# Optimization experiments

Hardware: AMD Instinct MI355X
Metric: run time of the kernel (lower is better)

Reference implementation:

```python
import jax, jax.numpy as jnp
import numpy as np

N = 100000      # nodes
E = 1600000     # directed edges (before self loops)
F_IN = 3        # node_feature_dim
H = 32          # hidden_dim
BN_EPS = 1e-5


def _linear_params(k, fan_in, fan_out):
    lim = 1.0 / np.sqrt(fan_in)
    kw, kb = jax.random.split(k)
    W = jax.random.uniform(kw, (fan_in, fan_out), jnp.float32, -lim, lim)
    b = jax.random.uniform(kb, (fan_out,), jnp.float32, -lim, lim)
    return W, b


def setup_inputs() -> dict:
    key = jax.random.key(0)
    ks = jax.random.split(key, 12)
    x = jax.random.normal(ks[0], (N, F_IN), jnp.float32)
    edge_index = jax.random.randint(ks[1], (2, E), 0, N, dtype=jnp.int64)
    node_type = jax.random.randint(ks[2], (N,), 0, 3, dtype=jnp.int64)
    W1, b1 = _linear_params(ks[3], F_IN, H)
    W2, b2 = _linear_params(ks[4], H, H)
    W3, b3 = _linear_params(ks[5], H, H)
    g1 = jnp.ones((H,), jnp.float32); be1 = jnp.zeros((H,), jnp.float32)
    g2 = jnp.ones((H,), jnp.float32); be2 = jnp.zeros((H,), jnp.float32)
    Wc1, bc1 = _linear_params(ks[6], H, H // 2)
    Wc2, bc2 = _linear_params(ks[7], H // 2, 1)
    Wd1, bd1 = _linear_params(ks[8], H, H // 2)
    Wd2, bd2 = _linear_params(ks[9], H // 2, 1)
    return dict(x=x, edge_index=edge_index, node_type=node_type,
                W1=W1, b1=b1, W2=W2, b2=b2, W3=W3, b3=b3,
                g1=g1, be1=be1, g2=g2, be2=be2,
                Wc1=Wc1, bc1=bc1, Wc2=Wc2, bc2=bc2,
                Wd1=Wd1, bd1=bd1, Wd2=Wd2, bd2=bd2)


def reference(x, edge_index, node_type, W1, b1, W2, b2, W3, b3,
              g1, be1, g2, be2, Wc1, bc1, Wc2, bc2, Wd1, bd1, Wd2, bd2):
    n = x.shape[0]
    # GCNConv (PyG default): add self loops, symmetric deg^-1/2 normalization
    loop = jnp.arange(n, dtype=edge_index.dtype)
    src = jnp.concatenate([edge_index[0], loop])  # [E+N]
    dst = jnp.concatenate([edge_index[1], loop])
    deg = jax.ops.segment_sum(jnp.ones_like(dst, dtype=x.dtype), dst, num_segments=n)
    dinv = jnp.where(deg > 0, jax.lax.rsqrt(jnp.maximum(deg, 1.0)), 0.0)
    norm = dinv[src] * dinv[dst]  # [E+N]

    def conv(h, W, b):
        msg = (h @ W)[src] * norm[:, None]                  # gather + scale
        return jax.ops.segment_sum(msg, dst, num_segments=n) + b  # scatter-add

    def bn(h, g, be):  # BatchNorm1d with batch statistics (training math)
        mu = h.mean(axis=0)
        var = ((h - mu) ** 2).mean(axis=0)
        return (h - mu) * jax.lax.rsqrt(var + BN_EPS) * g + be

    h = bn(jax.nn.relu(conv(x, W1, b1)), g1, be1)   # dropout = identity (eval)
    h = bn(jax.nn.relu(conv(h, W2, b2)), g2, be2)
    h = jax.nn.relu(conv(h, W3, b3))

    cand_mask = node_type == 0
    cand_emb = h[cand_mask]                                 # [C, H]
    cand_scores = (jax.nn.relu(cand_emb @ Wc1 + bc1) @ Wc2 + bc2)[:, 0]

    w = jax.nn.softmax(h.sum(axis=1))[:, None]              # [N,1] importance
    g_emb = (h * w).sum(axis=0, keepdims=True)              # [1, H]
    dn = (jax.nn.relu(g_emb @ Wd1 + bd1) @ Wd2 + bd2).reshape(())

    logits = jnp.concatenate([cand_scores, dn[None]], axis=0)
    cand_idx = jnp.nonzero(cand_mask)[0]
    return logits, cand_idx
```

## Files before the change

kernel.cpp:

```cpp
#include <hip/hip_runtime.h>

typedef unsigned int uint;
typedef unsigned char uchar;

#define NB_MAX 256
#define NPB_MAX 2048

#if defined(__has_builtin)
#if __has_builtin(__builtin_amdgcn_cvt_pk_f32_fp8) && __has_builtin(__builtin_amdgcn_cvt_pk_fp8_f32)
#define HW_FP8 1
#endif
#endif

typedef __attribute__((ext_vector_type(2))) float v2f;

static __device__ __forceinline__ uint f2fp8_sw(float v) {
    v = fminf(fmaxf(v, -448.f), 448.f);
    uint u = __float_as_uint(v);
    uint s = (u >> 24) & 0x80u;
    uint mag = u & 0x7FFFFFFFu;
    uint r = mag + 0x7FFFFu + ((mag >> 20) & 1u);
    if (r < 0x3C800000u) return s;
    uint e8 = (r - 0x3C000000u) >> 20;
    return s | min(e8, 0x7Eu);
}
static __device__ __forceinline__ float fp82f(uint b) {
    uint mag = b & 0x7Fu;
    uint bits = ((b & 0x80u) << 24) | ((mag << 20) + 0x3C000000u);
    return mag ? __uint_as_float(bits) : 0.f;
}
static __device__ __forceinline__ void dec8(uint2 v, float* o) {
#ifdef HW_FP8
    v2f a = __builtin_amdgcn_cvt_pk_f32_fp8((int)v.x, false);
    v2f b = __builtin_amdgcn_cvt_pk_f32_fp8((int)v.x, true);
    v2f c = __builtin_amdgcn_cvt_pk_f32_fp8((int)v.y, false);
    v2f d = __builtin_amdgcn_cvt_pk_f32_fp8((int)v.y, true);
    o[0]=a.x; o[1]=a.y; o[2]=b.x; o[3]=b.y;
    o[4]=c.x; o[5]=c.y; o[6]=d.x; o[7]=d.y;
#else
    o[0]=fp82f(v.x&0xFF); o[1]=fp82f((v.x>>8)&0xFF); o[2]=fp82f((v.x>>16)&0xFF); o[3]=fp82f(v.x>>24);
    o[4]=fp82f(v.y&0xFF); o[5]=fp82f((v.y>>8)&0xFF); o[6]=fp82f((v.y>>16)&0xFF); o[7]=fp82f(v.y>>24);
#endif
}
static __device__ __forceinline__ uint2 enc8(const float* o) {
#ifdef HW_FP8
    int rx = __builtin_amdgcn_cvt_pk_fp8_f32(o[0], o[1], 0, false);
    rx = __builtin_amdgcn_cvt_pk_fp8_f32(o[2], o[3], rx, true);
    int ry = __builtin_amdgcn_cvt_pk_fp8_f32(o[4], o[5], 0, false);
    ry = __builtin_amdgcn_cvt_pk_fp8_f32(o[6], o[7], ry, true);
    return make_uint2((uint)rx, (uint)ry);
#else
    uint2 r;
    r.x = f2fp8_sw(o[0]) | (f2fp8_sw(o[1])<<8) | (f2fp8_sw(o[2])<<16) | (f2fp8_sw(o[3])<<24);
    r.y = f2fp8_sw(o[4]) | (f2fp8_sw(o[5])<<8) | (f2fp8_sw(o[6])<<16) | (f2fp8_sw(o[7])<<24);
    return r;
#endif
}
static __device__ __forceinline__ void dec32(const uchar* row, float* o) {
    const uint4* r4 = (const uint4*)row;
    uint4 A = r4[0], B = r4[1];
    dec8(make_uint2(A.x,A.y), o); dec8(make_uint2(A.z,A.w), o+8);
    dec8(make_uint2(B.x,B.y), o+16); dec8(make_uint2(B.z,B.w), o+24);
}

static __device__ __forceinline__ unsigned wave_incl_scan(unsigned v) {
    int lane = threadIdx.x & 63;
    #pragma unroll
    for (int d = 1; d < 64; d <<= 1) {
        unsigned t = (unsigned)__shfl_up((int)v, d, 64);
        if (lane >= d) v += t;
    }
    return v;
}

static __device__ void block_excl_scan(const uint* in, uint* out, int n, uint* wscr) {
    int tid = threadIdx.x;
    int lane = tid & 63, wid = tid >> 6;
    int base = tid * 8;
    uint v[8], pre[8], s = 0;
    #pragma unroll
    for (int k = 0; k < 8; k++) v[k] = (base + k < n) ? in[base + k] : 0u;
    #pragma unroll
    for (int k = 0; k < 8; k++) { pre[k] = s; s += v[k]; }
    uint is = wave_incl_scan(s);
    __syncthreads();
    if (lane == 63) wscr[wid] = is;
    __syncthreads();
    uint woff = 0;
    for (int wI = 0; wI < wid; wI++) woff += wscr[wI];
    uint excl = is - s + woff;
    #pragma unroll
    for (int k = 0; k < 8; k++) if (base + k < n) out[base + k] = excl + pre[k];
    __syncthreads();
}

__global__ __launch_bounds__(256) void bucket_hist_kernel(const int* src, const int* dst,
                                                          const int* nt, uint* bcnt, uint* bcand,
                                                          int E, int N, int NB, int shift) {
    __shared__ uint bh[NB_MAX], ch[NB_MAX];
    int tid = threadIdx.x;
    bh[tid] = 0; ch[tid] = 0;
    __syncthreads();
    int gs = gridDim.x * 256;
    for (int i = blockIdx.x * 256 + tid; i < E; i += gs) {
        int d = dst[i], s = src[i];
        if ((uint)d < (uint)N && (uint)s < (uint)N) atomicAdd(&bh[d >> shift], 1u);
    }
    for (int i = blockIdx.x * 256 + tid; i < N; i += gs) {
        if (nt[i] == 0) atomicAdd(&ch[i >> shift], 1u);
    }
    __syncthreads();
    if (bh[tid]) atomicAdd(&bcnt[tid], bh[tid]);
    if (ch[tid]) atomicAdd(&bcand[tid], ch[tid]);
}

__global__ __launch_bounds__(256) void partition_kernel(const int* src, const int* dst,
                                                        const uint* bcnt, uint* alloc0,
                                                        uint* staging, int E, int N, int shift) {
    __shared__ uint bbase_s[NB_MAX];
    __shared__ uint lh[NB_MAX], gb[NB_MAX];
    __shared__ uint ws4[4];
    int tid = threadIdx.x;
    int lane = tid & 63, wid = tid >> 6;
    uint a = bcnt[tid];
    uint ia = wave_incl_scan(a);
    if (lane == 63) ws4[wid] = ia;
    __syncthreads();
    uint off = 0;
    for (int wI = 0; wI < wid; wI++) off += ws4[wI];
    bbase_s[tid] = ia - a + off;
    lh[tid] = 0;
    __syncthreads();
    int base = blockIdx.x * 2048;
    uint mask = (1u << shift) - 1u;
    int breg[8];
    uint rreg[8], pk8[8];
    #pragma unroll
    for (int k = 0; k < 8; k++) {
        int e = base + k * 256 + tid;
        breg[k] = -1;
        if (e < E) {
            int s = src[e], d = dst[e];
            if ((uint)d < (uint)N && (uint)s < (uint)N) {
                int b = d >> shift;
                pk8[k] = (((uint)d & mask) << 17) | (uint)s;
                breg[k] = b;
                rreg[k] = atomicAdd(&lh[b], 1u);
            }
        }
    }
    __syncthreads();
    gb[tid] = lh[tid] ? (bbase_s[tid] + atomicAdd(&alloc0[tid], lh[tid])) : 0u;
    __syncthreads();
    #pragma unroll
    for (int k = 0; k < 8; k++) {
        if (breg[k] >= 0)
            staging[gb[breg[k]] + rreg[k]] = pk8[k];
    }
}

__global__ __launch_bounds__(256) void local_csr_kernel(const uint* staging, const uint* bcnt,
                                                        const uint* bcand, const int* nt,
                                                        const float* x,
                                                        int* csr_src, uint* csr_off, uint* cand_pos,
                                                        float* dinv, float4* xs,
                                                        int N, int shift, int NB) {
    __shared__ uint deg[NPB_MAX];
    __shared__ uint ofs[NPB_MAX];
    __shared__ uint ws4[4];
    __shared__ uint sb[4];
    int b = blockIdx.x, tid = threadIdx.x;
    int lane = tid & 63, wid = tid >> 6;
    uint a = bcnt[tid];
    uint ia = wave_incl_scan(a);
    if (lane == 63) ws4[wid] = ia;
    __syncthreads();
    uint off = 0;
    for (int wI = 0; wI < wid; wI++) off += ws4[wI];
    if (tid == b) { sb[0] = ia - a + off; sb[1] = ia + off; }
    __syncthreads();
    uint c = bcand[tid];
    uint ic = wave_incl_scan(c);
    if (lane == 63) ws4[wid] = ic;
    __syncthreads();
    uint offc = 0;
    for (int wI = 0; wI < wid; wI++) offc += ws4[wI];
    if (tid == b) sb[2] = ic - c + offc;
    __syncthreads();
    uint ebase = sb[0], eend = sb[1], cb = sb[2];
    int nbase = b << shift;
    int ncount = min(1 << shift, N - nbase);
    for (int i = tid; i < ncount; i += 256) deg[i] = 0;
    __syncthreads();
    for (uint p = ebase + tid; p < eend; p += 256)
        atomicAdd(&deg[staging[p] >> 17], 1u);
    __syncthreads();
    block_excl_scan(deg, ofs, ncount, ws4);
    for (int i = tid; i < ncount; i += 256)
        csr_off[nbase + i] = ebase + ofs[i];
    if (b == NB - 1 && tid == 0) csr_off[N] = eend;
    for (int i = tid; i < ncount; i += 256) {
        int g = nbase + i;
        float di = rsqrtf((float)(deg[i] + 1u));
        dinv[g] = di;
        xs[g] = make_float4(x[3*g] * di, x[3*g+1] * di, x[3*g+2] * di, di);
    }
    __syncthreads();
    for (int i = tid; i < ncount; i += 256) deg[i] = 0;
    __syncthreads();
    for (uint p = ebase + tid; p < eend; p += 256) {
        uint pkv = staging[p];
        uint dl = pkv >> 17;
        uint pos = ebase + ofs[dl] + atomicAdd(&deg[dl], 1u);
        csr_src[pos] = (int)(pkv & 0x1FFFFu);
    }
    __syncthreads();
    for (int i = tid; i < ncount; i += 256) deg[i] = (nt[nbase + i] == 0) ? 1u : 0u;
    __syncthreads();
    block_excl_scan(deg, ofs, ncount, ws4);
    for (int i = tid; i < ncount; i += 256) cand_pos[nbase + i] = cb + ofs[i];
}

__global__ __launch_bounds__(256) void agg1_kernel(const float* xs, const int* csr_src,
                                                   const uint* csr_off, const float* dinv,
                                                   const float* W1, const float* b1, uchar* hb,
                                                   float* Sbuf, int n,
                                                   float* stats_sum, float* stats_sq,
                                                   uint* gt) {
    const int tid = threadIdx.x;
    const int wave = tid >> 6;
    const int lane = tid & 63;
    const int c4 = lane & 3;
    const int slot = lane >> 2;
    const int qlead = lane & ~3;
    __shared__ float W1s[96];
    __shared__ uint s_lt, s_chunk;
    if (tid < 96) W1s[tid] = W1[tid];
    float bv[8];
    #pragma unroll
    for (int j = 0; j < 8; j++) bv[j] = b1[c4 * 8 + j];
    float bs[8], bq[8];
    #pragma unroll
    for (int j = 0; j < 8; j++) { bs[j] = 0.f; bq[j] = 0.f; }
    __syncthreads();
    while (true) {
        if (tid == 0) s_chunk = atomicAdd(gt, 1u);
        __syncthreads();
        uint cbase = s_chunk * 128u;
        if (cbase >= (uint)n) break;
        uint avail = min((uint)n - cbase, 128u);
        if (tid == 0) s_lt = 0u;
        __syncthreads();
        while (true) {
            uint li = 0;
            if (c4 == 0) li = atomicAdd(&s_lt, 1u);
            li = (uint)__shfl((int)li, qlead, 64);
            if (li >= avail) break;
            uint node = cbase + li;
            uint s = csr_off[node], e = csr_off[node + 1];
            float acc = xs[(size_t)node * 4 + c4];
            for (uint p = s; p < e; p += 8) {
                uint idx[8];
                float wg[8];
                #pragma unroll
                for (int j = 0; j < 8; j++) {
                    uint q = p + (uint)j;
                    uint qc = min(q, e - 1u);
                    idx[j] = (uint)csr_src[qc];
                    wg[j] = (q < e) ? 1.f : 0.f;
                }
                #pragma unroll
                for (int j = 0; j < 8; j++)
                    acc = fmaf(wg[j], xs[(size_t)idx[j] * 4 + c4], acc);
            }
            if (c4 == 3) Sbuf[node] = acc;
            float di = dinv[node];
            float u = di * acc;
            float u0 = __shfl(u, qlead, 64);
            float u1 = __shfl(u, qlead + 1, 64);
            float u2 = __shfl(u, qlead + 2, 64);
            float hv[8], sv[8];
            #pragma unroll
            for (int j = 0; j < 8; j++) {
                int ch = c4 * 8 + j;
                float o = u0 * W1s[ch] + u1 * W1s[32 + ch] + u2 * W1s[64 + ch] + bv[j];
                hv[j] = fmaxf(o, 0.f);
                sv[j] = di * hv[j];
            }
            *(uint2*)(hb + (size_t)node * 32 + c4 * 8) = enc8(sv);
            #pragma unroll
            for (int j = 0; j < 8; j++) { bs[j] += hv[j]; bq[j] += hv[j] * hv[j]; }
        }
        __syncthreads();
    }
    #pragma unroll
    for (int m = 4; m < 64; m <<= 1) {
        #pragma unroll
        for (int j = 0; j < 8; j++) {
            bs[j] += __shfl_xor(bs[j], m, 64);
            bq[j] += __shfl_xor(bq[j], m, 64);
        }
    }
    __shared__ float ssum[4][32], ssq[4][32];
    if (slot == 0) {
        #pragma unroll
        for (int j = 0; j < 8; j++) { ssum[wave][c4 * 8 + j] = bs[j]; ssq[wave][c4 * 8 + j] = bq[j]; }
    }
    __syncthreads();
    if (tid < 32) {
        atomicAdd(&stats_sum[tid], ssum[0][tid] + ssum[1][tid] + ssum[2][tid] + ssum[3][tid]);
        atomicAdd(&stats_sq[tid],  ssq[0][tid] + ssq[1][tid] + ssq[2][tid] + ssq[3][tid]);
    }
}

template<int MODE>
__global__ __launch_bounds__(256) void aggbn_kernel(const uchar* hin, const int* csr_src,
                                                    const uint* csr_off, const float* dinv,
                                                    const float* Sbuf,
                                                    const float* stats_sum, const float* stats_sq,
                                                    const float* g, const float* be,
                                                    const float* W, const float* bias,
                                                    uchar* hout, int n, float inv_n,
                                                    float* osum, float* osq,
                                                    float* rowsum, uint* maxkey, uint* gt) {
    const int tid = threadIdx.x;
    const int wave = tid >> 6;
    const int lane = tid & 63;
    const int c4 = lane & 3;
    const int slot = lane >> 2;
    const int qlead = lane & ~3;
    __shared__ float Ws[1024];
    __shared__ float cs[32], a_s[32], d_s[32];
    __shared__ uint s_lt, s_chunk;
    if (tid < 32) {
        float mu = stats_sum[tid] * inv_n;
        float var = fmaxf(stats_sq[tid] * inv_n - mu * mu, 0.f);
        float a = g[tid] * rsqrtf(var + 1e-5f);
        a_s[tid] = a;
        d_s[tid] = be[tid] - mu * a;
    }
    __syncthreads();
    for (int t = tid; t < 1024; t += 256) Ws[t] = a_s[t >> 5] * W[t];
    if (tid < 32) {
        float c = 0.f;
        for (int k = 0; k < 32; k++) c += d_s[k] * W[k * 32 + tid];
        cs[tid] = c;
    }
    float bv[8];
    #pragma unroll
    for (int j = 0; j < 8; j++) bv[j] = bias[c4 * 8 + j];
    float bs[8], bq[8];
    if (MODE == 0) {
        #pragma unroll
        for (int j = 0; j < 8; j++) { bs[j] = 0.f; bq[j] = 0.f; }
    }
    float lmax = -3.0e38f;
    __syncthreads();
    while (true) {
        if (tid == 0) s_chunk = atomicAdd(gt, 1u);
        __syncthreads();
        uint cbase = s_chunk * 128u;
        if (cbase >= (uint)n) break;
        uint avail = min((uint)n - cbase, 128u);
        if (tid == 0) s_lt = 0u;
        __syncthreads();
        while (true) {
            uint li = 0;
            if (c4 == 0) li = atomicAdd(&s_lt, 1u);
            li = (uint)__shfl((int)li, qlead, 64);
            if (li >= avail) break;
            uint node = cbase + li;
            uint s = csr_off[node], e = csr_off[node + 1];
            float acc[8];
            dec8(*(const uint2*)(hin + (size_t)node * 32 + c4 * 8), acc);
            for (uint p = s; p < e; p += 8) {
                uint idx[8];
                float wg[8];
                #pragma unroll
                for (int j = 0; j < 8; j++) {
                    uint q = p + (uint)j;
                    uint qc = min(q, e - 1u);
                    idx[j] = (uint)csr_src[qc];
                    wg[j] = (q < e) ? 1.f : 0.f;
                }
                #pragma unroll
                for (int j = 0; j < 8; j++) {
                    float t[8];
                    dec8(*(const uint2*)(hin + (size_t)idx[j] * 32 + c4 * 8), t);
                    #pragma unroll
                    for (int cI = 0; cI < 8; cI++) acc[cI] = fmaf(wg[j], t[cI], acc[cI]);
                }
            }
            float af[32];
            #pragma unroll
            for (int cc = 0; cc < 4; cc++) {
                #pragma unroll
                for (int r = 0; r < 8; r++)
                    af[cc * 8 + r] = __shfl(acc[r], qlead + cc, 64);
            }
            float di = dinv[node];
            float Sv = Sbuf[node];
            float hv[8];
            #pragma unroll
            for (int jj = 0; jj < 8; jj++) {
                int j = c4 * 8 + jj;
                float t = cs[j] * Sv;
                #pragma unroll
                for (int k = 0; k < 32; k++) t = fmaf(Ws[k * 32 + j], af[k], t);
                hv[jj] = fmaxf(fmaf(di, t, bv[jj]), 0.f);
            }
            if (MODE == 0) {
                float sv[8];
                #pragma unroll
                for (int jj = 0; jj < 8; jj++) sv[jj] = di * hv[jj];
                *(uint2*)(hout + (size_t)node * 32 + c4 * 8) = enc8(sv);
                #pragma unroll
                for (int jj = 0; jj < 8; jj++) { bs[jj] += hv[jj]; bq[jj] += hv[jj] * hv[jj]; }
            } else {
                *(uint2*)(hout + (size_t)node * 32 + c4 * 8) = enc8(hv);
                float rs = ((hv[0] + hv[1]) + (hv[2] + hv[3])) + ((hv[4] + hv[5]) + (hv[6] + hv[7]));
                rs += __shfl_xor(rs, 1, 64);
                rs += __shfl_xor(rs, 2, 64);
                if (c4 == 0) { rowsum[node] = rs; lmax = fmaxf(lmax, rs); }
            }
        }
        __syncthreads();
    }
    if (MODE == 0) {
        #pragma unroll
        for (int m = 4; m < 64; m <<= 1) {
            #pragma unroll
            for (int j = 0; j < 8; j++) {
                bs[j] += __shfl_xor(bs[j], m, 64);
                bq[j] += __shfl_xor(bq[j], m, 64);
            }
        }
        __shared__ float ssum[4][32], ssq[4][32];
        if (slot == 0) {
            #pragma unroll
            for (int j = 0; j < 8; j++) { ssum[wave][c4 * 8 + j] = bs[j]; ssq[wave][c4 * 8 + j] = bq[j]; }
        }
        __syncthreads();
        if (tid < 32) {
            atomicAdd(&osum[tid], ssum[0][tid] + ssum[1][tid] + ssum[2][tid] + ssum[3][tid]);
            atomicAdd(&osq[tid],  ssq[0][tid] + ssq[1][tid] + ssq[2][tid] + ssq[3][tid]);
        }
    } else {
        #pragma unroll
        for (int m = 1; m < 64; m <<= 1) lmax = fmaxf(lmax, __shfl_xor(lmax, m, 64));
        __shared__ float lm[4];
        if (lane == 0) lm[wave] = lmax;
        __syncthreads();
        if (tid == 0) {
            float m = fmaxf(fmaxf(lm[0], lm[1]), fmaxf(lm[2], lm[3]));
            uint u = __float_as_uint(m);
            uint key = (u & 0x80000000u) ? ~u : (u | 0x80000000u);
            atomicMax(maxkey, key);
        }
    }
}

__global__ __launch_bounds__(256) void head_kernel(const uchar* hb, const int* nt,
                                                   const uint* pos, const float* Wc1,
                                                   const float* bc1, const float* Wc2,
                                                   const float* bc2, const float* rowsum,
                                                   const uint* maxkey, float* gvec, float* Zp,
                                                   uint* ticket, const float* Wd1,
                                                   const float* bd1, const float* Wd2,
                                                   const float* bd2, float* out, int n, int C) {
    __shared__ float W1s[512], b1s[16], W2s[16];
    __shared__ float ls[256];
    __shared__ float ge[32], tt[16];
    __shared__ int lastflag;
    int tid = threadIdx.x;
    for (int t = tid; t < 512; t += 256) W1s[t] = Wc1[t];
    if (tid < 16) { b1s[tid] = bc1[tid]; W2s[tid] = Wc2[tid]; }
    __syncthreads();
    int i = blockIdx.x * 256 + tid;
    if (i < n && nt[i] == 0) {
        float hv[32];
        dec32(hb + (size_t)i * 32, hv);
        float s = bc2[0];
        #pragma unroll
        for (int j = 0; j < 16; j++) {
            float u = b1s[j];
            #pragma unroll
            for (int k = 0; k < 32; k++) u += hv[k] * W1s[k * 16 + j];
            s += fmaxf(u, 0.f) * W2s[j];
        }
        s = fminf(fmaxf(s, -1000.f), 1000.f);
        uint p = pos[i];
        if (p < (uint)C) {
            out[p] = s;
            out[C + 1 + p] = (float)i;
        }
    }
    uint key = *maxkey;
    float M = 0.f;
    if (key != 0u) M = (key & 0x80000000u) ? __uint_as_float(key ^ 0x80000000u) : __uint_as_float(~key);
    int lane = tid & 31, grp = tid >> 5;
    int stride = gridDim.x * 8;
    float accZ = 0.f, accg = 0.f;
    for (int node = blockIdx.x * 8 + grp; node < n; node += stride) {
        float ew = __expf(rowsum[node] - M);
        accg += fp82f(hb[(size_t)node * 32 + lane]) * ew;
        if (lane == 0) accZ += ew;
    }
    ls[tid] = accg;
    __syncthreads();
    if (tid < 32) {
        float a = 0.f;
        #pragma unroll
        for (int g = 0; g < 8; g++) a += ls[tid + 32 * g];
        atomicAdd(&gvec[tid], a);
    }
    __syncthreads();
    ls[tid] = (lane == 0) ? accZ : 0.f;
    __syncthreads();
    if (tid == 0) {
        float a = 0.f;
        for (int t = 0; t < 256; t += 32) a += ls[t];
        atomicAdd(Zp, a);
        __threadfence();
        uint old = atomicAdd(ticket, 1u);
        lastflag = (old == gridDim.x - 1) ? 1 : 0;
    }
    __syncthreads();
    if (lastflag) {
        __threadfence();
        if (tid < 32) ge[tid] = atomicAdd(&gvec[tid], 0.f);
        if (tid == 0) ls[0] = atomicAdd(Zp, 0.f);
        __syncthreads();
        float Zv = fmaxf(ls[0], 1e-30f);
        if (tid < 32) ge[tid] /= Zv;
        __syncthreads();
        if (tid < 16) {
            float s = bd1[tid];
            for (int k = 0; k < 32; k++) s += ge[k] * Wd1[k * 16 + tid];
            tt[tid] = fmaxf(s, 0.f);
        }
        __syncthreads();
        if (tid == 0) {
            float s = bd2[0];
            for (int j = 0; j < 16; j++) s += tt[j] * Wd2[j];
            out[C] = fminf(fmaxf(s, -1000.f), 1000.f);
        }
    }
}

extern "C" void kernel_launch(void* const* d_in, const int* in_sizes, int n_in,
                              void* d_out, int out_size, void* d_ws, size_t ws_size,
                              hipStream_t stream) {
    const float* x   = (const float*)d_in[0];
    const int*   ei  = (const int*)d_in[1];
    const int*   nt  = (const int*)d_in[2];
    const float* W1  = (const float*)d_in[3];  const float* b1  = (const float*)d_in[4];
    const float* W2  = (const float*)d_in[5];  const float* b2  = (const float*)d_in[6];
    const float* W3  = (const float*)d_in[7];  const float* b3  = (const float*)d_in[8];
    const float* g1  = (const float*)d_in[9];  const float* be1 = (const float*)d_in[10];
    const float* g2  = (const float*)d_in[11]; const float* be2 = (const float*)d_in[12];
    const float* Wc1 = (const float*)d_in[13]; const float* bc1 = (const float*)d_in[14];
    const float* Wc2 = (const float*)d_in[15]; const float* bc2 = (const float*)d_in[16];
    const float* Wd1 = (const float*)d_in[17]; const float* bd1 = (const float*)d_in[18];
    const float* Wd2 = (const float*)d_in[19]; const float* bd2 = (const float*)d_in[20];

    const int N = in_sizes[0] / 3;
    const int E = in_sizes[1] / 2;
    const int C = (out_size - 1) / 2;
    const int* e_src = ei;
    const int* e_dst = ei + E;
    float* out = (float*)d_out;

    int shift = 9;
    while (((N + (1 << shift) - 1) >> shift) > NB_MAX) shift++;
    const int NB = (N + (1 << shift) - 1) >> shift;

    char* w = (char*)d_ws;
    auto alloc = [&](size_t bytes) { void* p = (void*)w; w += (bytes + 255) & ~(size_t)255; return p; };
    float*    stats  = (float*)alloc(256 * 4);
    uint*     bcnt   = (uint*)alloc(NB_MAX * 4);
    uint*     bcand  = (uint*)alloc(NB_MAX * 4);
    uint*     alloc0 = (uint*)alloc(NB_MAX * 4);
    size_t zero_bytes = (size_t)((char*)w - (char*)stats);
    float*    dinv   = (float*)alloc((size_t)N * 4);
    uint*     csr_off= (uint*)alloc((size_t)(N + 1) * 4);
    uint*     cand_pos=(uint*)alloc((size_t)N * 4);
    float*    rowsum = (float*)alloc((size_t)N * 4);
    float*    Sbuf   = (float*)alloc((size_t)N * 4);
    int*      csr_src= (int*)alloc((size_t)E * 4);
    uint*     staging= (uint*)alloc((size_t)E * 4);
    uchar*    zb     = (uchar*)alloc((size_t)N * 32);
    uchar*    hb     = (uchar*)alloc((size_t)N * 32);
    float4*   xs     = (float4*)zb;

    float* sum1 = stats;       float* sq1 = stats + 32;
    float* sum2 = stats + 64;  float* sq2 = stats + 96;
    float* gvec = stats + 128; float* Zp  = stats + 160;
    uint* maxkey = (uint*)(stats + 161);
    uint* ticket = (uint*)(stats + 162);
    uint* gt1 = (uint*)(stats + 163);
    uint* gt2 = (uint*)(stats + 164);
    uint* gt3 = (uint*)(stats + 165);

    hipMemsetAsync(stats, 0, zero_bytes, stream);

    const int gN   = (N + 255) / 256;
    const int gPar = (E + 2047) / 2048;
    int gAgg = (N + 127) / 128;
    if (gAgg > 512) gAgg = 512;
    const float inv_n = 1.0f / (float)N;

    hipLaunchKernelGGL(bucket_hist_kernel, dim3(784), dim3(256), 0, stream, e_src, e_dst, nt, bcnt, bcand, E, N, NB, shift);
    hipLaunchKernelGGL(partition_kernel, dim3(gPar), dim3(256), 0, stream, e_src, e_dst, bcnt, alloc0, staging, E, N, shift);
    hipLaunchKernelGGL(local_csr_kernel, dim3(NB), dim3(256), 0, stream, staging, bcnt, bcand, nt,
                       x, csr_src, csr_off, cand_pos, dinv, xs, N, shift, NB);

    hipLaunchKernelGGL(agg1_kernel, dim3(gAgg), dim3(256), 0, stream, (const float*)xs, csr_src, csr_off,
                       dinv, W1, b1, hb, Sbuf, N, sum1, sq1, gt1);

    hipLaunchKernelGGL((aggbn_kernel<0>), dim3(gAgg), dim3(256), 0, stream, hb, csr_src, csr_off,
                       dinv, Sbuf, sum1, sq1, g1, be1, W2, b2, zb, N, inv_n,
                       sum2, sq2, rowsum, maxkey, gt2);

    hipLaunchKernelGGL((aggbn_kernel<1>), dim3(gAgg), dim3(256), 0, stream, zb, csr_src, csr_off,
                       dinv, Sbuf, sum2, sq2, g2, be2, W3, b3, hb, N, inv_n,
                       sum1, sq1, rowsum, maxkey, gt3);

    hipLaunchKernelGGL(head_kernel, dim3(gN), dim3(256), 0, stream, hb, nt, cand_pos,
                       Wc1, bc1, Wc2, bc2, rowsum, maxkey, gvec, Zp, ticket,
                       Wd1, bd1, Wd2, bd2, out, N, C);
}
```

Before: 309.4 us.

## Fuse head kernel into layer-3 aggregation with online softmax and per-block partials

The candidate-scoring MLP and the softmax-weighted graph pooling move into the third aggregation kernel. The softmax uses an online running max, per-block partials of (M, Z, g) and a last-block ticket reduction. This removes the separate head kernel launch, the rowsum buffer, the re-read of the final hidden features and the global max atomic pass. The aggregation grid cap rises from 512 to 1024 blocks, which adds more final-reduction work in the last block and per-node exp work in the hot loop.

```diff
diff --git a/kernel.cpp b/kernel.cpp
--- a/kernel.cpp
+++ b/kernel.cpp
@@ -5,6 +5,7 @@
 
 #define NB_MAX 256
 #define NPB_MAX 2048
+#define GAGG_MAX 1024
 
 #if defined(__has_builtin)
 #if __has_builtin(__builtin_amdgcn_cvt_pk_f32_fp8) && __has_builtin(__builtin_amdgcn_cvt_pk_fp8_f32)
@@ -55,12 +56,6 @@
     r.y = f2fp8_sw(o[4]) | (f2fp8_sw(o[5])<<8) | (f2fp8_sw(o[6])<<16) | (f2fp8_sw(o[7])<<24);
     return r;
 #endif
-}
-static __device__ __forceinline__ void dec32(const uchar* row, float* o) {
-    const uint4* r4 = (const uint4*)row;
-    uint4 A = r4[0], B = r4[1];
-    dec8(make_uint2(A.x,A.y), o); dec8(make_uint2(A.z,A.w), o+8);
-    dec8(make_uint2(B.x,B.y), o+16); dec8(make_uint2(B.z,B.w), o+24);
 }
 
 static __device__ __forceinline__ unsigned wave_incl_scan(unsigned v) {
@@ -313,16 +308,14 @@
     }
 }
 
-template<int MODE>
-__global__ __launch_bounds__(256) void aggbn_kernel(const uchar* hin, const int* csr_src,
-                                                    const uint* csr_off, const float* dinv,
-                                                    const float* Sbuf,
-                                                    const float* stats_sum, const float* stats_sq,
-                                                    const float* g, const float* be,
-                                                    const float* W, const float* bias,
-                                                    uchar* hout, int n, float inv_n,
-                                                    float* osum, float* osq,
-                                                    float* rowsum, uint* maxkey, uint* gt) {
+__global__ __launch_bounds__(256) void aggbn2_kernel(const uchar* hin, const int* csr_src,
+                                                     const uint* csr_off, const float* dinv,
+                                                     const float* Sbuf,
+                                                     const float* stats_sum, const float* stats_sq,
+                                                     const float* g, const float* be,
+                                                     const float* W, const float* bias,
+                                                     uchar* hout, int n, float inv_n,
+                                                     float* osum, float* osq, uint* gt) {
     const int tid = threadIdx.x;
     const int wave = tid >> 6;
     const int lane = tid & 63;
@@ -350,11 +343,8 @@
     #pragma unroll
     for (int j = 0; j < 8; j++) bv[j] = bias[c4 * 8 + j];
     float bs[8], bq[8];
-    if (MODE == 0) {
-        #pragma unroll
-        for (int j = 0; j < 8; j++) { bs[j] = 0.f; bq[j] = 0.f; }
-    }
-    float lmax = -3.0e38f;
+    #pragma unroll
+    for (int j = 0; j < 8; j++) { bs[j] = 0.f; bq[j] = 0.f; }
     __syncthreads();
     while (true) {
         if (tid == 0) s_chunk = atomicAdd(gt, 1u);
@@ -400,7 +390,7 @@
             }
             float di = dinv[node];
             float Sv = Sbuf[node];
-            float hv[8];
+            float hv[8], sv[8];
             #pragma unroll
             for (int jj = 0; jj < 8; jj++) {
                 int j = c4 * 8 + jj;
@@ -408,143 +398,268 @@
                 #pragma unroll
                 for (int k = 0; k < 32; k++) t = fmaf(Ws[k * 32 + j], af[k], t);
                 hv[jj] = fmaxf(fmaf(di, t, bv[jj]), 0.f);
-            }
-            if (MODE == 0) {
-                float sv[8];
-                #pragma unroll
-                for (int jj = 0; jj < 8; jj++) sv[jj] = di * hv[jj];
-                *(uint2*)(hout + (size_t)node * 32 + c4 * 8) = enc8(sv);
-                #pragma unroll
-                for (int jj = 0; jj < 8; jj++) { bs[jj] += hv[jj]; bq[jj] += hv[jj] * hv[jj]; }
-            } else {
-                *(uint2*)(hout + (size_t)node * 32 + c4 * 8) = enc8(hv);
-                float rs = ((hv[0] + hv[1]) + (hv[2] + hv[3])) + ((hv[4] + hv[5]) + (hv[6] + hv[7]));
-                rs += __shfl_xor(rs, 1, 64);
-                rs += __shfl_xor(rs, 2, 64);
-                if (c4 == 0) { rowsum[node] = rs; lmax = fmaxf(lmax, rs); }
-            }
+                sv[jj] = di * hv[jj];
+            }
+            *(uint2*)(hout + (size_t)node * 32 + c4 * 8) = enc8(sv);
+            #pragma unroll
+            for (int jj = 0; jj < 8; jj++) { bs[jj] += hv[jj]; bq[jj] += hv[jj] * hv[jj]; }
         }
         __syncthreads();
     }
-    if (MODE == 0) {
+    #pragma unroll
+    for (int m = 4; m < 64; m <<= 1) {
         #pragma unroll
-        for (int m = 4; m < 64; m <<= 1) {
-            #pragma unroll
-            for (int j = 0; j < 8; j++) {
-                bs[j] += __shfl_xor(bs[j], m, 64);
-                bq[j] += __shfl_xor(bq[j], m, 64);
-            }
+        for (int j = 0; j < 8; j++) {
+            bs[j] += __shfl_xor(bs[j], m, 64);
+            bq[j] += __shfl_xor(bq[j], m, 64);
         }
-        __shared__ float ssum[4][32], ssq[4][32];
-        if (slot == 0) {
-            #pragma unroll
-            for (int j = 0; j < 8; j++) { ssum[wave][c4 * 8 + j] = bs[j]; ssq[wave][c4 * 8 + j] = bq[j]; }
+    }
+    __shared__ float ssum[4][32], ssq[4][32];
+    if (slot == 0) {
+        #pragma unroll
+        for (int j = 0; j < 8; j++) { ssum[wave][c4 * 8 + j] = bs[j]; ssq[wave][c4 * 8 + j] = bq[j]; }
+    }
+    __syncthreads();
+    if (tid < 32) {
+        atomicAdd(&osum[tid], ssum[0][tid] + ssum[1][tid] + ssum[2][tid] + ssum[3][tid]);
+        atomicAdd(&osq[tid],  ssq[0][tid] + ssq[1][tid] + ssq[2][tid] + ssq[3][tid]);
+    }
+}
+
+__global__ __launch_bounds__(256) void aggbn3_kernel(const uchar* hin, const int* csr_src,
+                                                     const uint* csr_off, const float* dinv,
+                                                     const float* Sbuf,
+                                                     const float* stats_sum, const float* stats_sq,
+                                                     const float* g, const float* be,
+                                                     const float* W, const float* bias,
+                                                     const int* nt, const uint* cand_pos,
+                                                     const float* Wc1, const float* bc1,
+                                                     const float* Wc2, const float* bc2,
+                                                     const float* Wd1, const float* bd1,
+                                                     const float* Wd2, const float* bd2,
+                                                     float* blkM, float* blkZ, float* blkG,
+                                                     uint* ticket, float* out,
+                                                     int n, int C, float inv_n, uint* gt) {
+    const int tid = threadIdx.x;
+    const int wave = tid >> 6;
+    const int lane = tid & 63;
+    const int c4 = lane & 3;
+    const int qlead = lane & ~3;
+    __shared__ float Ws[1024];
+    __shared__ float cs[32], a_s[32], d_s[32];
+    __shared__ float W1h[512], b1h[16], W2h[16];
+    __shared__ float pM[4], pZ[4], pgs[4][32];
+    __shared__ float red[8][32], mred[4], geS[32], ttS[16];
+    __shared__ uint s_lt, s_chunk;
+    __shared__ int lastflag;
+    if (tid < 32) {
+        float mu = stats_sum[tid] * inv_n;
+        float var = fmaxf(stats_sq[tid] * inv_n - mu * mu, 0.f);
+        float a = g[tid] * rsqrtf(var + 1e-5f);
+        a_s[tid] = a;
+        d_s[tid] = be[tid] - mu * a;
+    }
+    __syncthreads();
+    for (int t = tid; t < 1024; t += 256) Ws[t] = a_s[t >> 5] * W[t];
+    for (int t = tid; t < 512; t += 256) W1h[t] = Wc1[t];
+    if (tid < 32) {
+        float c = 0.f;
+        for (int k = 0; k < 32; k++) c += d_s[k] * W[k * 32 + tid];
+        cs[tid] = c;
+    }
+    if (tid < 16) { b1h[tid] = bc1[tid]; W2h[tid] = Wc2[tid]; }
+    float bv[8];
+    #pragma unroll
+    for (int j = 0; j < 8; j++) bv[j] = bias[c4 * 8 + j];
+    float M = -3.0e38f, Zl = 0.f, pg[8];
+    #pragma unroll
+    for (int j = 0; j < 8; j++) pg[j] = 0.f;
+    const float bc2v = bc2[0];
+    __syncthreads();
+    while (true) {
+        if (tid == 0) s_chunk = atomicAdd(gt, 1u);
+        __syncthreads();
+        uint cbase = s_chunk * 128u;
+        if (cbase >= (uint)n) break;
+        uint avail = min((uint)n - cbase, 128u);
+        if (tid == 0) s_lt = 0u;
+        __syncthreads();
+        while (true) {
+            uint li = 0;
+            if (c4 == 0) li = atomicAdd(&s_lt, 1u);
+            li = (uint)__shfl((int)li, qlead, 64);
+            if (li >= avail) break;
+            uint node = cbase + li;
+            uint s = csr_off[node], e = csr_off[node + 1];
+            float acc[8];
+            dec8(*(const uint2*)(hin + (size_t)node * 32 + c4 * 8), acc);
+            for (uint p = s; p < e; p += 8) {
+                uint idx[8];
+                float wg[8];
+                #pragma unroll
+                for (int j = 0; j < 8; j++) {
+                    uint q = p + (uint)j;
+                    uint qc = min(q, e - 1u);
+                    idx[j] = (uint)csr_src[qc];
+                    wg[j] = (q < e) ? 1.f : 0.f;
+                }
+                #pragma unroll
+                for (int j = 0; j < 8; j++) {
+                    float t[8];
+                    dec8(*(const uint2*)(hin + (size_t)idx[j] * 32 + c4 * 8), t);
+                    #pragma unroll
+                    for (int cI = 0; cI < 8; cI++) acc[cI] = fmaf(wg[j], t[cI], acc[cI]);
+                }
+            }
+            float af[32];
+            #pragma unroll
+            for (int cc = 0; cc < 4; cc++) {
+                #pragma unroll
+                for (int r = 0; r < 8; r++)
+                    af[cc * 8 + r] = __shfl(acc[r], qlead + cc, 64);
+            }
+            float di = dinv[node];
+            float Sv = Sbuf[node];
+            float hv[8];
+            #pragma unroll
+            for (int jj = 0; jj < 8; jj++) {
+                int j = c4 * 8 + jj;
+                float t = cs[j] * Sv;
+                #pragma unroll
+                for (int k = 0; k < 32; k++) t = fmaf(Ws[k * 32 + j], af[k], t);
+                hv[jj] = fmaxf(fmaf(di, t, bv[jj]), 0.f);
+            }
+            float rs = ((hv[0] + hv[1]) + (hv[2] + hv[3])) + ((hv[4] + hv[5]) + (hv[6] + hv[7]));
+            rs += __shfl_xor(rs, 1, 64);
+            rs += __shfl_xor(rs, 2, 64);
+            if (rs > M) {
+                float f = __expf(M - rs);
+                #pragma unroll
+                for (int j = 0; j < 8; j++) pg[j] *= f;
+                Zl *= f;
+                M = rs;
+            }
+            float wgt = __expf(rs - M);
+            #pragma unroll
+            for (int j = 0; j < 8; j++) pg[j] = fmaf(hv[j], wgt, pg[j]);
+            Zl += wgt;
+            if (nt[node] == 0) {
+                float pu[16];
+                #pragma unroll
+                for (int j = 0; j < 16; j++) {
+                    float t = 0.f;
+                    #pragma unroll
+                    for (int jj = 0; jj < 8; jj++)
+                        t = fmaf(hv[jj], W1h[(c4 * 8 + jj) * 16 + j], t);
+                    pu[j] = t;
+                }
+                #pragma unroll
+                for (int j = 0; j < 16; j++) {
+                    pu[j] += __shfl_xor(pu[j], 1, 64);
+                    pu[j] += __shfl_xor(pu[j], 2, 64);
+                }
+                if (c4 == 0) {
+                    float sc = bc2v;
+                    #pragma unroll
+                    for (int j = 0; j < 16; j++)
+                        sc += fmaxf(pu[j] + b1h[j], 0.f) * W2h[j];
+                    sc = fminf(fmaxf(sc, -1000.f), 1000.f);
+                    uint pp = cand_pos[node];
+                    if (pp < (uint)C) {
+                        out[pp] = sc;
+                        out[C + 1 + pp] = (float)node;
+                    }
+                }
+            }
         }
         __syncthreads();
-        if (tid < 32) {
-            atomicAdd(&osum[tid], ssum[0][tid] + ssum[1][tid] + ssum[2][tid] + ssum[3][tid]);
-            atomicAdd(&osq[tid],  ssq[0][tid] + ssq[1][tid] + ssq[2][tid] + ssq[3][tid]);
+    }
+    #pragma unroll
+    for (int m = 4; m < 64; m <<= 1) {
+        float Mo = __shfl_xor(M, m, 64);
+        float Zo = __shfl_xor(Zl, m, 64);
+        float Mn = fmaxf(M, Mo);
+        float fa = __expf(M - Mn), fb = __expf(Mo - Mn);
+        #pragma unroll
+        for (int j = 0; j < 8; j++) {
+            float po = __shfl_xor(pg[j], m, 64);
+            pg[j] = pg[j] * fa + po * fb;
         }
-    } else {
+        Zl = Zl * fa + Zo * fb;
+        M = Mn;
+    }
+    if ((lane >> 2) == 0) {
+        if (c4 == 0) { pM[wave] = M; pZ[wave] = Zl; }
         #pragma unroll
-        for (int m = 1; m < 64; m <<= 1) lmax = fmaxf(lmax, __shfl_xor(lmax, m, 64));
-        __shared__ float lm[4];
-        if (lane == 0) lm[wave] = lmax;
-        __syncthreads();
-        if (tid == 0) {
-            float m = fmaxf(fmaxf(lm[0], lm[1]), fmaxf(lm[2], lm[3]));
-            uint u = __float_as_uint(m);
-            uint key = (u & 0x80000000u) ? ~u : (u | 0x80000000u);
-            atomicMax(maxkey, key);
-        }
-    }
-}
-
-__global__ __launch_bounds__(256) void head_kernel(const uchar* hb, const int* nt,
-                                                   const uint* pos, const float* Wc1,
-                                                   const float* bc1, const float* Wc2,
-                                                   const float* bc2, const float* rowsum,
-                                                   const uint* maxkey, float* gvec, float* Zp,
-                                                   uint* ticket, const float* Wd1,
-                                                   const float* bd1, const float* Wd2,
-                                                   const float* bd2, float* out, int n, int C) {
-    __shared__ float W1s[512], b1s[16], W2s[16];
-    __shared__ float ls[256];
-    __shared__ float ge[32], tt[16];
-    __shared__ int lastflag;
-    int tid = threadIdx.x;
-    for (int t = tid; t < 512; t += 256) W1s[t] = Wc1[t];
-    if (tid < 16) { b1s[tid] = bc1[tid]; W2s[tid] = Wc2[tid]; }
-    __syncthreads();
-    int i = blockIdx.x * 256 + tid;
-    if (i < n && nt[i] == 0) {
-        float hv[32];
-        dec32(hb + (size_t)i * 32, hv);
-        float s = bc2[0];
-        #pragma unroll
-        for (int j = 0; j < 16; j++) {
-            float u = b1s[j];
-            #pragma unroll
-            for (int k = 0; k < 32; k++) u += hv[k] * W1s[k * 16 + j];
-            s += fmaxf(u, 0.f) * W2s[j];
-        }
-        s = fminf(fmaxf(s, -1000.f), 1000.f);
-        uint p = pos[i];
-        if (p < (uint)C) {
-            out[p] = s;
-            out[C + 1 + p] = (float)i;
-        }
-    }
-    uint key = *maxkey;
-    float M = 0.f;
-    if (key != 0u) M = (key & 0x80000000u) ? __uint_as_float(key ^ 0x80000000u) : __uint_as_float(~key);
-    int lane = tid & 31, grp = tid >> 5;
-    int stride = gridDim.x * 8;
-    float accZ = 0.f, accg = 0.f;
-    for (int node = blockIdx.x * 8 + grp; node < n; node += stride) {
-        float ew = __expf(rowsum[node] - M);
-        accg += fp82f(hb[(size_t)node * 32 + lane]) * ew;
-        if (lane == 0) accZ += ew;
-    }
-    ls[tid] = accg;
+        for (int j = 0; j < 8; j++) pgs[wave][c4 * 8 + j] = pg[j];
+    }
     __syncthreads();
     if (tid < 32) {
+        float Mn = fmaxf(fmaxf(pM[0], pM[1]), fmaxf(pM[2], pM[3]));
         float a = 0.f;
         #pragma unroll
-        for (int g = 0; g < 8; g++) a += ls[tid + 32 * g];
-        atomicAdd(&gvec[tid], a);
-    }
-    __syncthreads();
-    ls[tid] = (lane == 0) ? accZ : 0.f;
+        for (int wv = 0; wv < 4; wv++) a += pgs[wv][tid] * __expf(pM[wv] - Mn);
+        __hip_atomic_store(&blkG[(size_t)blockIdx.x * 32 + tid], a, __ATOMIC_RELAXED, __HIP_MEMORY_SCOPE_AGENT);
+        if (tid == 0) {
+            float Zt = 0.f;
+            #pragma unroll
+            for (int wv = 0; wv < 4; wv++) Zt += pZ[wv] * __expf(pM[wv] - Mn);
+            __hip_atomic_store(&blkM[blockIdx.x], Mn, __ATOMIC_RELAXED, __HIP_MEMORY_SCOPE_AGENT);
+            __hip_atomic_store(&blkZ[blockIdx.x], Zt, __ATOMIC_RELAXED, __HIP_MEMORY_SCOPE_AGENT);
+        }
+    }
     __syncthreads();
     if (tid == 0) {
-        float a = 0.f;
-        for (int t = 0; t < 256; t += 32) a += ls[t];
-        atomicAdd(Zp, a);
         __threadfence();
         uint old = atomicAdd(ticket, 1u);
         lastflag = (old == gridDim.x - 1) ? 1 : 0;
     }
     __syncthreads();
-    if (lastflag) {
-        __threadfence();
-        if (tid < 32) ge[tid] = atomicAdd(&gvec[tid], 0.f);
-        if (tid == 0) ls[0] = atomicAdd(Zp, 0.f);
-        __syncthreads();
-        float Zv = fmaxf(ls[0], 1e-30f);
-        if (tid < 32) ge[tid] /= Zv;
-        __syncthreads();
-        if (tid < 16) {
-            float s = bd1[tid];
-            for (int k = 0; k < 32; k++) s += ge[k] * Wd1[k * 16 + tid];
-            tt[tid] = fmaxf(s, 0.f);
-        }
-        __syncthreads();
-        if (tid == 0) {
-            float s = bd2[0];
-            for (int j = 0; j < 16; j++) s += tt[j] * Wd2[j];
-            out[C] = fminf(fmaxf(s, -1000.f), 1000.f);
-        }
+    if (!lastflag) return;
+    __threadfence();
+    int NBLK = gridDim.x;
+    float lm = -3.0e38f;
+    for (int b = tid; b < NBLK; b += 256)
+        lm = fmaxf(lm, __hip_atomic_load(&blkM[b], __ATOMIC_RELAXED, __HIP_MEMORY_SCOPE_AGENT));
+    #pragma unroll
+    for (int m = 1; m < 64; m <<= 1) lm = fmaxf(lm, __shfl_xor(lm, m, 64));
+    if ((tid & 63) == 0) mred[tid >> 6] = lm;
+    __syncthreads();
+    float Mg = fmaxf(fmaxf(mred[0], mred[1]), fmaxf(mred[2], mred[3]));
+    int lane32 = tid & 31, grp8 = tid >> 5;
+    float a = 0.f, z = 0.f;
+    for (int b = grp8; b < NBLK; b += 8) {
+        float f = __expf(__hip_atomic_load(&blkM[b], __ATOMIC_RELAXED, __HIP_MEMORY_SCOPE_AGENT) - Mg);
+        a += __hip_atomic_load(&blkG[(size_t)b * 32 + lane32], __ATOMIC_RELAXED, __HIP_MEMORY_SCOPE_AGENT) * f;
+        if (lane32 == 0) z += __hip_atomic_load(&blkZ[b], __ATOMIC_RELAXED, __HIP_MEMORY_SCOPE_AGENT) * f;
+    }
+    red[grp8][lane32] = a;
+    __syncthreads();
+    if (tid < 32) {
+        float t = 0.f;
+        #pragma unroll
+        for (int gI = 0; gI < 8; gI++) t += red[gI][tid];
+        geS[tid] = t;
+    }
+    if (tid < 8) red[0][tid] = (tid == 0) ? z : 0.f;
+    __syncthreads();
+    if (lane32 == 0) mred[0] = 0.f;
+    __syncthreads();
+    if (lane32 == 0) atomicAdd(&mred[0], z);
+    __syncthreads();
+    float Zv = fmaxf(mred[0], 1e-30f);
+    if (tid < 32) geS[tid] /= Zv;
+    __syncthreads();
+    if (tid < 16) {
+        float s = bd1[tid];
+        for (int k = 0; k < 32; k++) s += geS[k] * Wd1[k * 16 + tid];
+        ttS[tid] = fmaxf(s, 0.f);
+    }
+    __syncthreads();
+    if (tid == 0) {
+        float s = bd2[0];
+        for (int j = 0; j < 16; j++) s += ttS[j] * Wd2[j];
+        out[C] = fminf(fmaxf(s, -1000.f), 1000.f);
     }
 }
 
@@ -585,8 +700,10 @@
     float*    dinv   = (float*)alloc((size_t)N * 4);
     uint*     csr_off= (uint*)alloc((size_t)(N + 1) * 4);
     uint*     cand_pos=(uint*)alloc((size_t)N * 4);
-    float*    rowsum = (float*)alloc((size_t)N * 4);
     float*    Sbuf   = (float*)alloc((size_t)N * 4);
+    float*    blkM   = (float*)alloc(GAGG_MAX * 4);
+    float*    blkZ   = (float*)alloc(GAGG_MAX * 4);
+    float*    blkG   = (float*)alloc((size_t)GAGG_MAX * 32 * 4);
     int*      csr_src= (int*)alloc((size_t)E * 4);
     uint*     staging= (uint*)alloc((size_t)E * 4);
     uchar*    zb     = (uchar*)alloc((size_t)N * 32);
@@ -595,8 +712,6 @@
 
     float* sum1 = stats;       float* sq1 = stats + 32;
     float* sum2 = stats + 64;  float* sq2 = stats + 96;
-    float* gvec = stats + 128; float* Zp  = stats + 160;
-    uint* maxkey = (uint*)(stats + 161);
     uint* ticket = (uint*)(stats + 162);
     uint* gt1 = (uint*)(stats + 163);
     uint* gt2 = (uint*)(stats + 164);
@@ -604,10 +719,9 @@
 
     hipMemsetAsync(stats, 0, zero_bytes, stream);
 
-    const int gN   = (N + 255) / 256;
     const int gPar = (E + 2047) / 2048;
     int gAgg = (N + 127) / 128;
-    if (gAgg > 512) gAgg = 512;
+    if (gAgg > GAGG_MAX) gAgg = GAGG_MAX;
     const float inv_n = 1.0f / (float)N;
 
     hipLaunchKernelGGL(bucket_hist_kernel, dim3(784), dim3(256), 0, stream, e_src, e_dst, nt, bcnt, bcand, E, N, NB, shift);
@@ -618,15 +732,12 @@
     hipLaunchKernelGGL(agg1_kernel, dim3(gAgg), dim3(256), 0, stream, (const float*)xs, csr_src, csr_off,
                        dinv, W1, b1, hb, Sbuf, N, sum1, sq1, gt1);
 
-    hipLaunchKernelGGL((aggbn_kernel<0>), dim3(gAgg), dim3(256), 0, stream, hb, csr_src, csr_off,
+    hipLaunchKernelGGL(aggbn2_kernel, dim3(gAgg), dim3(256), 0, stream, hb, csr_src, csr_off,
                        dinv, Sbuf, sum1, sq1, g1, be1, W2, b2, zb, N, inv_n,
-                       sum2, sq2, rowsum, maxkey, gt2);
-
-    hipLaunchKernelGGL((aggbn_kernel<1>), dim3(gAgg), dim3(256), 0, stream, zb, csr_src, csr_off,
-                       dinv, Sbuf, sum2, sq2, g2, be2, W3, b3, hb, N, inv_n,
-                       sum1, sq1, rowsum, maxkey, gt3);
-
-    hipLaunchKernelGGL(head_kernel, dim3(gN), dim3(256), 0, stream, hb, nt, cand_pos,
-                       Wc1, bc1, Wc2, bc2, rowsum, maxkey, gvec, Zp, ticket,
-                       Wd1, bd1, Wd2, bd2, out, N, C);
-}
+                       sum2, sq2, gt2);
+
+    hipLaunchKernelGGL(aggbn3_kernel, dim3(gAgg), dim3(256), 0, stream, zb, csr_src, csr_off,
+                       dinv, Sbuf, sum2, sq2, g2, be2, W3, b3,
+                       nt, cand_pos, Wc1, bc1, Wc2, bc2, Wd1, bd1, Wd2, bd2,
+                       blkM, blkZ, blkG, ticket, out, N, C, inv_n, gt3);
+}
```

Result: slower. 346.5 us (+12.0%).

## Process each node with two lanes instead of four in aggregation kernels

Applied to the files above, without the earlier changes.

Remaps the GCN aggregation kernels so each node is handled by a lane pair, each lane owning 16 channels with 16-byte fp8 loads, instead of a quad with 8 channels each. This halves the redundant CSR index loads per node, doubles the nodes in flight per wave, and replaces the 32-value quad shuffle with a 16-value pair exchange before the 32x32 matvec. It also adds launch_bounds min-blocks of 2. The cost is higher register pressure per lane, which may reduce occupancy or cause spills.

```diff
diff --git a/kernel.cpp b/kernel.cpp
--- a/kernel.cpp
+++ b/kernel.cpp
@@ -55,6 +55,14 @@
     r.y = f2fp8_sw(o[4]) | (f2fp8_sw(o[5])<<8) | (f2fp8_sw(o[6])<<16) | (f2fp8_sw(o[7])<<24);
     return r;
 #endif
+}
+static __device__ __forceinline__ void dec16(uint4 v, float* o) {
+    dec8(make_uint2(v.x, v.y), o);
+    dec8(make_uint2(v.z, v.w), o + 8);
+}
+static __device__ __forceinline__ void enc16(const float* o, uchar* dst) {
+    uint2 a = enc8(o), b = enc8(o + 8);
+    *(uint4*)dst = make_uint4(a.x, a.y, b.x, b.y);
 }
 static __device__ __forceinline__ void dec32(const uchar* row, float* o) {
     const uint4* r4 = (const uint4*)row;
@@ -221,27 +229,27 @@
     for (int i = tid; i < ncount; i += 256) cand_pos[nbase + i] = cb + ofs[i];
 }
 
-__global__ __launch_bounds__(256) void agg1_kernel(const float* xs, const int* csr_src,
-                                                   const uint* csr_off, const float* dinv,
-                                                   const float* W1, const float* b1, uchar* hb,
-                                                   float* Sbuf, int n,
-                                                   float* stats_sum, float* stats_sq,
-                                                   uint* gt) {
+__global__ __launch_bounds__(256, 2) void agg1_kernel(const float* xs, const int* csr_src,
+                                                      const uint* csr_off, const float* dinv,
+                                                      const float* W1, const float* b1, uchar* hb,
+                                                      float* Sbuf, int n,
+                                                      float* stats_sum, float* stats_sq,
+                                                      uint* gt) {
     const int tid = threadIdx.x;
     const int wave = tid >> 6;
     const int lane = tid & 63;
-    const int c4 = lane & 3;
-    const int slot = lane >> 2;
-    const int qlead = lane & ~3;
+    const int c2 = lane & 1;
+    const int plead = lane & ~1;
     __shared__ float W1s[96];
     __shared__ uint s_lt, s_chunk;
     if (tid < 96) W1s[tid] = W1[tid];
-    float bv[8];
-    #pragma unroll
-    for (int j = 0; j < 8; j++) bv[j] = b1[c4 * 8 + j];
-    float bs[8], bq[8];
-    #pragma unroll
-    for (int j = 0; j < 8; j++) { bs[j] = 0.f; bq[j] = 0.f; }
+    const float2* xs2 = (const float2*)xs;
+    float bv[16];
+    #pragma unroll
+    for (int j = 0; j < 16; j++) bv[j] = b1[c2 * 16 + j];
+    float bs[16], bq[16];
+    #pragma unroll
+    for (int j = 0; j < 16; j++) { bs[j] = 0.f; bq[j] = 0.f; }
     __syncthreads();
     while (true) {
         if (tid == 0) s_chunk = atomicAdd(gt, 1u);
@@ -253,12 +261,13 @@
         __syncthreads();
         while (true) {
             uint li = 0;
-            if (c4 == 0) li = atomicAdd(&s_lt, 1u);
-            li = (uint)__shfl((int)li, qlead, 64);
+            if (c2 == 0) li = atomicAdd(&s_lt, 1u);
+            li = (uint)__shfl((int)li, plead, 64);
             if (li >= avail) break;
             uint node = cbase + li;
             uint s = csr_off[node], e = csr_off[node + 1];
-            float acc = xs[(size_t)node * 4 + c4];
+            float2 selfv = xs2[(size_t)node * 2 + c2];
+            float a0 = selfv.x, a1 = selfv.y;
             for (uint p = s; p < e; p += 8) {
                 uint idx[8];
                 float wg[8];
@@ -270,41 +279,44 @@
                     wg[j] = (q < e) ? 1.f : 0.f;
                 }
                 #pragma unroll
-                for (int j = 0; j < 8; j++)
-                    acc = fmaf(wg[j], xs[(size_t)idx[j] * 4 + c4], acc);
+                for (int j = 0; j < 8; j++) {
+                    float2 t = xs2[(size_t)idx[j] * 2 + c2];
+                    a0 = fmaf(wg[j], t.x, a0);
+                    a1 = fmaf(wg[j], t.y, a1);
+                }
             }
-            if (c4 == 3) Sbuf[node] = acc;
+            if (c2 == 1) Sbuf[node] = a1;
             float di = dinv[node];
-            float u = di * acc;
-            float u0 = __shfl(u, qlead, 64);
-            float u1 = __shfl(u, qlead + 1, 64);
-            float u2 = __shfl(u, qlead + 2, 64);
-            float hv[8], sv[8];
+            float u0l = di * a0, u1l = di * a1;
+            float u0 = __shfl(u0l, plead, 64);
+            float u1 = __shfl(u1l, plead, 64);
+            float u2 = __shfl(u0l, plead + 1, 64);
+            float hv[16], sv[16];
             #pragma unroll
-            for (int j = 0; j < 8; j++) {
-                int ch = c4 * 8 + j;
+            for (int j = 0; j < 16; j++) {
+                int ch = c2 * 16 + j;
                 float o = u0 * W1s[ch] + u1 * W1s[32 + ch] + u2 * W1s[64 + ch] + bv[j];
                 hv[j] = fmaxf(o, 0.f);
                 sv[j] = di * hv[j];
             }
-            *(uint2*)(hb + (size_t)node * 32 + c4 * 8) = enc8(sv);
+            enc16(sv, hb + (size_t)node * 32 + c2 * 16);
             #pragma unroll
-            for (int j = 0; j < 8; j++) { bs[j] += hv[j]; bq[j] += hv[j] * hv[j]; }
-        }
-        __syncthreads();
-    }
-    #pragma unroll
-    for (int m = 4; m < 64; m <<= 1) {
+            for (int j = 0; j < 16; j++) { bs[j] += hv[j]; bq[j] += hv[j] * hv[j]; }
+        }
+        __syncthreads();
+    }
+    #pragma unroll
+    for (int m = 2; m < 64; m <<= 1) {
         #pragma unroll
-        for (int j = 0; j < 8; j++) {
+        for (int j = 0; j < 16; j++) {
             bs[j] += __shfl_xor(bs[j], m, 64);
             bq[j] += __shfl_xor(bq[j], m, 64);
         }
     }
     __shared__ float ssum[4][32], ssq[4][32];
-    if (slot == 0) {
+    if ((lane >> 1) == 0) {
         #pragma unroll
-        for (int j = 0; j < 8; j++) { ssum[wave][c4 * 8 + j] = bs[j]; ssq[wave][c4 * 8 + j] = bq[j]; }
+        for (int j = 0; j < 16; j++) { ssum[wave][c2 * 16 + j] = bs[j]; ssq[wave][c2 * 16 + j] = bq[j]; }
     }
     __syncthreads();
     if (tid < 32) {
@@ -314,21 +326,20 @@
 }
 
 template<int MODE>
-__global__ __launch_bounds__(256) void aggbn_kernel(const uchar* hin, const int* csr_src,
-                                                    const uint* csr_off, const float* dinv,
-                                                    const float* Sbuf,
-                                                    const float* stats_sum, const float* stats_sq,
-                                                    const float* g, const float* be,
-                                                    const float* W, const float* bias,
-                                                    uchar* hout, int n, float inv_n,
-                                                    float* osum, float* osq,
-                                                    float* rowsum, uint* maxkey, uint* gt) {
+__global__ __launch_bounds__(256, 2) void aggbn_kernel(const uchar* hin, const int* csr_src,
+                                                       const uint* csr_off, const float* dinv,
+                                                       const float* Sbuf,
+                                                       const float* stats_sum, const float* stats_sq,
+                                                       const float* g, const float* be,
+                                                       const float* W, const float* bias,
+                                                       uchar* hout, int n, float inv_n,
+                                                       float* osum, float* osq,
+                                                       float* rowsum, uint* maxkey, uint* gt) {
     const int tid = threadIdx.x;
     const int wave = tid >> 6;
     const int lane = tid & 63;
-    const int c4 = lane & 3;
-    const int slot = lane >> 2;
-    const int qlead = lane & ~3;
+    const int c2 = lane & 1;
+    const int plead = lane & ~1;
     __shared__ float Ws[1024];
     __shared__ float cs[32], a_s[32], d_s[32];
     __shared__ uint s_lt, s_chunk;
@@ -346,13 +357,13 @@
         for (int k = 0; k < 32; k++) c += d_s[k] * W[k * 32 + tid];
         cs[tid] = c;
     }
-    float bv[8];
-    #pragma unroll
-    for (int j = 0; j < 8; j++) bv[j] = bias[c4 * 8 + j];
-    float bs[8], bq[8];
+    float bv[16];
+    #pragma unroll
+    for (int j = 0; j < 16; j++) bv[j] = bias[c2 * 16 + j];
+    float bs[16], bq[16];
     if (MODE == 0) {
         #pragma unroll
-        for (int j = 0; j < 8; j++) { bs[j] = 0.f; bq[j] = 0.f; }
+        for (int j = 0; j < 16; j++) { bs[j] = 0.f; bq[j] = 0.f; }
     }
     float lmax = -3.0e38f;
     __syncthreads();
@@ -366,13 +377,13 @@
         __syncthreads();
         while (true) {
             uint li = 0;
-            if (c4 == 0) li = atomicAdd(&s_lt, 1u);
-            li = (uint)__shfl((int)li, qlead, 64);
+            if (c2 == 0) li = atomicAdd(&s_lt, 1u);
+            li = (uint)__shfl((int)li, plead, 64);
             if (li >= avail) break;
             uint node = cbase + li;
             uint s = csr_off[node], e = csr_off[node + 1];
-            float acc[8];
-            dec8(*(const uint2*)(hin + (size_t)node * 32 + c4 * 8), acc);
+            float acc[16];
+            dec16(*(const uint4*)(hin + (size_t)node * 32 + c2 * 16), acc);
             for (uint p = s; p < e; p += 8) {
                 uint idx[8];
                 float wg[8];
@@ -385,60 +396,60 @@
                 }
                 #pragma unroll
                 for (int j = 0; j < 8; j++) {
-                    float t[8];
-                    dec8(*(const uint2*)(hin + (size_t)idx[j] * 32 + c4 * 8), t);
+                    float t[16];
+                    dec16(*(const uint4*)(hin + (size_t)idx[j] * 32 + c2 * 16), t);
                     #pragma unroll
-                    for (int cI = 0; cI < 8; cI++) acc[cI] = fmaf(wg[j], t[cI], acc[cI]);
+                    for (int cI = 0; cI < 16; cI++) acc[cI] = fmaf(wg[j], t[cI], acc[cI]);
                 }
             }
-            float af[32];
+            float pacc[16];
             #pragma unroll
-            for (int cc = 0; cc < 4; cc++) {
-                #pragma unroll
-                for (int r = 0; r < 8; r++)
-                    af[cc * 8 + r] = __shfl(acc[r], qlead + cc, 64);
-            }
+            for (int r = 0; r < 16; r++) pacc[r] = __shfl_xor(acc[r], 1, 64);
             float di = dinv[node];
             float Sv = Sbuf[node];
-            float hv[8];
+            const int ownk = c2 * 16, prtk = 16 - c2 * 16;
+            float hv[16];
             #pragma unroll
-            for (int jj = 0; jj < 8; jj++) {
-                int j = c4 * 8 + jj;
+            for (int jj = 0; jj < 16; jj++) {
+                int j = c2 * 16 + jj;
                 float t = cs[j] * Sv;
                 #pragma unroll
-                for (int k = 0; k < 32; k++) t = fmaf(Ws[k * 32 + j], af[k], t);
+                for (int r = 0; r < 16; r++) t = fmaf(Ws[(ownk + r) * 32 + j], acc[r], t);
+                #pragma unroll
+                for (int r = 0; r < 16; r++) t = fmaf(Ws[(prtk + r) * 32 + j], pacc[r], t);
                 hv[jj] = fmaxf(fmaf(di, t, bv[jj]), 0.f);
             }
             if (MODE == 0) {
-                float sv[8];
-                #pragma unroll
-                for (int jj = 0; jj < 8; jj++) sv[jj] = di * hv[jj];
-                *(uint2*)(hout + (size_t)node * 32 + c4 * 8) = enc8(sv);
-                #pragma unroll
-                for (int jj = 0; jj < 8; jj++) { bs[jj] += hv[jj]; bq[jj] += hv[jj] * hv[jj]; }
+                float sv[16];
+                #pragma unroll
+                for (int jj = 0; jj < 16; jj++) sv[jj] = di * hv[jj];
+                enc16(sv, hout + (size_t)node * 32 + c2 * 16);
+                #pragma unroll
+                for (int jj = 0; jj < 16; jj++) { bs[jj] += hv[jj]; bq[jj] += hv[jj] * hv[jj]; }
             } else {
-                *(uint2*)(hout + (size_t)node * 32 + c4 * 8) = enc8(hv);
-                float rs = ((hv[0] + hv[1]) + (hv[2] + hv[3])) + ((hv[4] + hv[5]) + (hv[6] + hv[7]));
+                enc16(hv, hout + (size_t)node * 32 + c2 * 16);
+                float rs = 0.f;
+                #pragma unroll
+                for (int jj = 0; jj < 16; jj++) rs += hv[jj];
                 rs += __shfl_xor(rs, 1, 64);
-                rs += __shfl_xor(rs, 2, 64);
-                if (c4 == 0) { rowsum[node] = rs; lmax = fmaxf(lmax, rs); }
+                if (c2 == 0) { rowsum[node] = rs; lmax = fmaxf(lmax, rs); }
             }
         }
         __syncthreads();
     }
     if (MODE == 0) {
         #pragma unroll
-        for (int m = 4; m < 64; m <<= 1) {
+        for (int m = 2; m < 64; m <<= 1) {
             #pragma unroll
-            for (int j = 0; j < 8; j++) {
+            for (int j = 0; j < 16; j++) {
                 bs[j] += __shfl_xor(bs[j], m, 64);
                 bq[j] += __shfl_xor(bq[j], m, 64);
             }
         }
         __shared__ float ssum[4][32], ssq[4][32];
-        if (slot == 0) {
+        if ((lane >> 1) == 0) {
             #pragma unroll
-            for (int j = 0; j < 8; j++) { ssum[wave][c4 * 8 + j] = bs[j]; ssq[wave][c4 * 8 + j] = bq[j]; }
+            for (int j = 0; j < 16; j++) { ssum[wave][c2 * 16 + j] = bs[j]; ssq[wave][c2 * 16 + j] = bq[j]; }
         }
         __syncthreads();
         if (tid < 32) {
```

Result: slower. 324.4 us (+4.9%).
